# Kernel optimization log

Hardware: AMD Instinct MI355X
Metric: run time of the kernel (lower is better)

## Reference

```python
import jax, jax.numpy as jnp
import numpy as np

N_HEADS = 16
WINDOW = 4
THETA = 10000.0


def _freqs_1d(dim, L, theta=THETA):
    f = 1.0 / theta ** (np.arange(0, dim, 2, dtype=np.float32) / dim)  # [dim/2]
    ang = np.arange(L, dtype=np.float32)[:, None] * f[None, :]         # [L, dim/2]
    return jnp.asarray(np.cos(ang)), jnp.asarray(np.sin(ang))


def _freqs_2d(dim, H, W, theta=THETA):
    f = 1.0 / theta ** (np.arange(0, dim, 2, dtype=np.float32) / dim)  # [dim/2]
    fh = np.arange(H, dtype=np.float32)[:, None] * f[0::2][None, :]    # [H, dim/4]
    fw = np.arange(W, dtype=np.float32)[:, None] * f[1::2][None, :]    # [W, dim/4]
    ang = np.concatenate([
        np.broadcast_to(fh[:, None, :], (H, W, fh.shape[1])),
        np.broadcast_to(fw[None, :, :], (H, W, fw.shape[1])),
    ], axis=-1)                                                        # [H, W, dim/2]
    return jnp.asarray(np.cos(ang)), jnp.asarray(np.sin(ang))


def _rope(x, cos, sin):
    # x: [..., N, D]; cos/sin broadcastable to x's leading dims with trailing D/2
    sh = x.shape
    xr = x.reshape(sh[:-1] + (sh[-1] // 2, 2))
    re, im = xr[..., 0], xr[..., 1]
    o_re = re * cos - im * sin
    o_im = re * sin + im * cos
    return jnp.stack([o_re, o_im], axis=-1).reshape(sh)


def setup_inputs() -> dict:
    key = jax.random.key(0)
    ks = jax.random.split(key, 5)
    B, T, H, W, E = 2, 8, 16, 16, 512
    S = 2 * T * H * W
    std = 0.02
    return {
        "hidden_states": jax.random.normal(ks[0], (B, S, E), jnp.float32),
        "in_proj_weight": jax.random.normal(ks[1], (3 * E, E), jnp.float32) * std,
        "in_proj_bias": jnp.zeros((3 * E,), jnp.float32),
        "out_proj_weight": jax.random.normal(ks[2], (E, E), jnp.float32) * std,
        "out_proj_bias": jnp.zeros((E,), jnp.float32),
        "temporal_embed": jax.random.normal(ks[3], (WINDOW, E), jnp.float32) * std,
        "T": T, "H": H, "W": W,
    }


def reference(hidden_states, in_proj_weight, in_proj_bias, out_proj_weight,
              out_proj_bias, temporal_embed, T, H, W):
    B, S, E = hidden_states.shape
    n, d = N_HEADS, E // N_HEADS
    HW = H * W
    THW = T * HW
    L2 = 2 * HW  # tokens per frame fed to attention

    # first (outer) in-projection
    qkv = hidden_states @ in_proj_weight.T + in_proj_bias  # [B,S,3E]
    q, k, v = jnp.split(qkv, 3, axis=-1)
    q = q.reshape(B, S, n, d)
    k = k.reshape(B, S, n, d)

    # 1D RoPE on first T*H*W tokens (per-frame length H*W)
    cos1, sin1 = _freqs_1d(d, HW)
    c1, s1 = cos1[:, None, :], sin1[:, None, :]  # [HW,1,d/2]
    q1 = _rope(q[:, :THW].reshape(B * T, HW, n, d), c1, s1)
    k1 = _rope(k[:, :THW].reshape(B * T, HW, n, d), c1, s1)

    # 2D RoPE on last T*H*W tokens
    cos2, sin2 = _freqs_2d(d, H, W)
    c2, s2 = cos2[:, :, None, :], sin2[:, :, None, :]  # [H,W,1,d/2]
    q2 = _rope(q[:, THW:].reshape(B * T, H, W, n, d), c2, s2).reshape(B * T, HW, n, d)
    k2 = _rope(k[:, THW:].reshape(B * T, H, W, n, d), c2, s2).reshape(B * T, HW, n, d)

    q_mha = jnp.concatenate([q1, q2], axis=1).reshape(B * T, L2, E)
    k_comb = jnp.concatenate([k1, k2], axis=1).reshape(B, T, L2, E)
    v_comb = v.reshape(B, T, L2, E)

    # sliding window over frames (left-pad with zeros)
    k_pad = jnp.pad(k_comb, ((0, 0), (WINDOW - 1, 0), (0, 0), (0, 0)))
    v_pad = jnp.pad(v_comb, ((0, 0), (WINDOW - 1, 0), (0, 0), (0, 0)))
    k_win = jnp.stack([k_pad[:, i:i + T] for i in range(WINDOW)], axis=2)
    v_win = jnp.stack([v_pad[:, i:i + T] for i in range(WINDOW)], axis=2)
    k_win = k_win + temporal_embed[None, None, :, None, :]
    k_mha = k_win.reshape(B * T, WINDOW * L2, E)
    v_mha = v_win.reshape(B * T, WINDOW * L2, E)

    # inner nn.MultiheadAttention: projects q/k/v AGAIN with in_proj chunks
    Wq, Wk, Wv = jnp.split(in_proj_weight, 3, axis=0)
    bq, bk, bv = jnp.split(in_proj_bias, 3, axis=0)
    qh = (q_mha @ Wq.T + bq).reshape(B * T, L2, n, d)
    kh = (k_mha @ Wk.T + bk).reshape(B * T, WINDOW * L2, n, d)
    vh = (v_mha @ Wv.T + bv).reshape(B * T, WINDOW * L2, n, d)

    scale = 1.0 / jnp.sqrt(jnp.asarray(d, jnp.float32))
    scores = jnp.einsum('bqnd,bknd->bnqk', qh, kh) * scale
    attn = jax.nn.softmax(scores, axis=-1)
    o = jnp.einsum('bnqk,bknd->bqnd', attn, vh).reshape(B * T, L2, E)
    out = o @ out_proj_weight.T + out_proj_bias
    return out.reshape(B, S, E)
```

## Files before the change

### kernel.cpp

```cpp
#include <hip/hip_runtime.h>


#define LOG2T_OVER_16 0.83048202372184059f
#define SCL 0.25505837391169026f

typedef unsigned short u16;
typedef unsigned int u32;
typedef __attribute__((ext_vector_type(2))) unsigned int u32x2;
typedef __attribute__((ext_vector_type(4))) float f32x4;
typedef __attribute__((ext_vector_type(8))) short s16x8;

__device__ __forceinline__ u16 bf16b(float x) {
  u32 u = __float_as_uint(x);
  u32 r = u + 0x7FFFu + ((u >> 16) & 1u);
  return (u16)(r >> 16);
}
__device__ __forceinline__ float bf2f(u16 s) {
  return __uint_as_float(((u32)s) << 16);
}

__device__ __forceinline__ void gld_lds16(const u16* g, u16* l) {
  __builtin_amdgcn_global_load_lds(
      (const __attribute__((address_space(1))) unsigned int*)g,
      (__attribute__((address_space(3))) unsigned int*)l, 16, 0, 0);
}

__global__ __launch_bounds__(256) void cast_bf16(
    const float* __restrict__ src, u16* __restrict__ dst, int n8) {
  int i = blockIdx.x * 256 + threadIdx.x;
  if (i >= n8) return;
  float4 a = ((const float4*)src)[i * 2], b = ((const float4*)src)[i * 2 + 1];
  s16x8 w;
  w[0] = (short)bf16b(a.x); w[1] = (short)bf16b(a.y);
  w[2] = (short)bf16b(a.z); w[3] = (short)bf16b(a.w);
  w[4] = (short)bf16b(b.x); w[5] = (short)bf16b(b.y);
  w[6] = (short)bf16b(b.z); w[7] = (short)bf16b(b.w);
  ((s16x8*)dst)[i] = w;
}

template<int OUTF32>
__device__ __forceinline__ void gemm_core(
    const u16* __restrict__ A, const u16* __restrict__ Bw,
    const float* __restrict__ bias, void* __restrict__ Cp,
    int N, int K, float scale, u16* As, u16* Bs) {
  const int tid = threadIdx.x;
  const int row0 = blockIdx.y * 128;
  const int col0 = blockIdx.x * 128;
  const int lane = tid & 63, wid = tid >> 6;
  const int col = lane & 15, g = lane >> 4;
  const int wm = wid >> 1, wn = wid & 1;

  const int s0 = tid, s1 = 256 + tid;
  const int r0 = s0 >> 2, kp0 = (s0 & 3) * 8;
  const int r1 = s1 >> 2, kp1 = (s1 & 3) * 8;

  f32x4 acc[4][4] = {};

  auto stage = [&](int buf, int k0) {
    u16* ab = As + buf * 4096;
    u16* bb = Bs + buf * 4096;
    gld_lds16(A + (size_t)(row0 + r0) * K + k0 + kp0, ab + s0 * 8);
    gld_lds16(A + (size_t)(row0 + r1) * K + k0 + kp1, ab + s1 * 8);
    gld_lds16(Bw + (size_t)(col0 + r0) * K + k0 + kp0, bb + s0 * 8);
    gld_lds16(Bw + (size_t)(col0 + r1) * K + k0 + kp1, bb + s1 * 8);
  };

  stage(0, 0);
  asm volatile("s_waitcnt vmcnt(0)" ::: "memory");
  __syncthreads();

  const int NT = K / 32;
  int cur = 0;
  for (int t = 0; t < NT; ++t) {
    if (t + 1 < NT) stage(cur ^ 1, (t + 1) * 32);
    const u16* ab = As + cur * 4096;
    const u16* bb = Bs + cur * 4096;
    s16x8 a[4], b[4];
    #pragma unroll
    for (int i = 0; i < 4; ++i)
      a[i] = *(const s16x8*)(ab + (wm * 64 + i * 16 + col) * 32 + g * 8);
    #pragma unroll
    for (int i = 0; i < 4; ++i)
      b[i] = *(const s16x8*)(bb + (wn * 64 + i * 16 + col) * 32 + g * 8);
    #pragma unroll
    for (int mi = 0; mi < 4; ++mi)
      #pragma unroll
      for (int ni = 0; ni < 4; ++ni)
        acc[mi][ni] = __builtin_amdgcn_mfma_f32_16x16x32_bf16(a[mi], b[ni], acc[mi][ni], 0, 0, 0);
    asm volatile("s_waitcnt vmcnt(0)" ::: "memory");
    __syncthreads();
    cur ^= 1;
  }

  const int crow = row0 + wm * 64, ccol = col0 + wn * 64;
  #pragma unroll
  for (int mi = 0; mi < 4; ++mi) {
    #pragma unroll
    for (int ni = 0; ni < 4; ++ni) {
      const int cc = ccol + ni * 16 + col;
      const float bb_ = bias ? bias[cc] : 0.0f;
      #pragma unroll
      for (int r = 0; r < 4; ++r) {
        const int rr = crow + mi * 16 + g * 4 + r;
        float v = (acc[mi][ni][r] + bb_) * scale;
        if (OUTF32) ((float*)Cp)[(size_t)rr * N + cc] = v;
        else        ((u16*)Cp)[(size_t)rr * N + cc] = bf16b(v);
      }
    }
  }
}

__global__ __launch_bounds__(256) void gemm_bf16(
    const u16* __restrict__ A, const u16* __restrict__ Bw,
    const float* __restrict__ bias, u16* __restrict__ C, int N, int K, float scale) {
  __shared__ u16 As[2 * 4096];
  __shared__ u16 Bs[2 * 4096];
  gemm_core<0>(A, Bw, bias, C, N, K, scale, As, Bs);
}

__global__ __launch_bounds__(256) void gemm_f32out(
    const u16* __restrict__ A, const u16* __restrict__ Bw,
    const float* __restrict__ bias, float* __restrict__ C, int N, int K, float scale) {
  __shared__ u16 As[2 * 4096];
  __shared__ u16 Bs[2 * 4096];
  gemm_core<1>(A, Bw, bias, C, N, K, scale, As, Bs);
}

__global__ __launch_bounds__(256) void gemm2_batched(
    const u16* __restrict__ Ab, const u16* __restrict__ Wb,
    const float* __restrict__ b_in, u16* __restrict__ Cb) {
  __shared__ u16 As[2 * 4096];
  __shared__ u16 Bs[2 * 4096];
  const int z = blockIdx.z;
  const u16* A  = Ab + (size_t)z * 4194304;
  const u16* Bw = Wb + (size_t)z * 262144;
  u16* C = Cb + (size_t)z * 4194304;
  const float* bias = (z == 0) ? b_in : (z == 2 ? b_in + 1024 : nullptr);
  const float scale = (z == 0) ? SCL : 1.0f;
  gemm_core<0>(A, Bw, bias, C, 512, 512, scale, As, Bs);
}

__global__ __launch_bounds__(256) void rope_relayout_bf(
    const u16* __restrict__ qkv, u16* __restrict__ qm,
    u16* __restrict__ kc, u16* __restrict__ vc) {
  const int R = blockIdx.x * 2 + (threadIdx.x >> 7);
  const int t2 = threadIdx.x & 127;
  const int j = R & 511, bt = R >> 9;
  const int b = bt >> 3, tt = bt & 7;
  const int head = t2 >> 3, u0 = (t2 & 7) * 2;
  const int e0 = head * 32 + u0 * 2;

  float ang0, ang1; int tok;
  if (j < 256) {
    ang0 = (float)j * exp2f(-(float)u0 * LOG2T_OVER_16);
    ang1 = (float)j * exp2f(-(float)(u0 + 1) * LOG2T_OVER_16);
    tok = b * 4096 + tt * 256 + j;
  } else {
    const int jj = j - 256, hh = jj >> 4, ww = jj & 15;
    ang0 = (u0 < 8) ? (float)hh * exp2f(-(float)(2 * u0) * LOG2T_OVER_16)
                    : (float)ww * exp2f(-(float)(2 * (u0 - 8) + 1) * LOG2T_OVER_16);
    const int u1 = u0 + 1;
    ang1 = (u1 < 8) ? (float)hh * exp2f(-(float)(2 * u1) * LOG2T_OVER_16)
                    : (float)ww * exp2f(-(float)(2 * (u1 - 8) + 1) * LOG2T_OVER_16);
    tok = b * 4096 + 2048 + tt * 256 + jj;
  }
  float s0, c0, s1, c1;
  sincosf(ang0, &s0, &c0);
  sincosf(ang1, &s1, &c1);

  const size_t base = (size_t)tok * 1536 + e0;
  const size_t orow = (size_t)R * 512 + e0;

  auto rot = [&](u32x2 in) -> u32x2 {
    float r0 = bf2f((u16)(in[0] & 0xffff)), i0 = bf2f((u16)(in[0] >> 16));
    float r1 = bf2f((u16)(in[1] & 0xffff)), i1 = bf2f((u16)(in[1] >> 16));
    u32x2 o;
    o[0] = (u32)bf16b(r0 * c0 - i0 * s0) | ((u32)bf16b(r0 * s0 + i0 * c0) << 16);
    o[1] = (u32)bf16b(r1 * c1 - i1 * s1) | ((u32)bf16b(r1 * s1 + i1 * c1) << 16);
    return o;
  };
  *(u32x2*)(qm + orow) = rot(*(const u32x2*)(qkv + base));
  *(u32x2*)(kc + orow) = rot(*(const u32x2*)(qkv + base + 512));
  const int vtok = b * 4096 + tt * 512 + j;
  *(u32x2*)(vc + orow) = *(const u32x2*)(qkv + (size_t)vtok * 1536 + 1024 + e0);
}

__global__ __launch_bounds__(256) void tep_kernel(
    const float* __restrict__ te, const float* __restrict__ Wk,
    const float* __restrict__ bk, float* __restrict__ tep) {
  const int idx = blockIdx.x * 256 + threadIdx.x;
  const int i = idx >> 9, c = idx & 511;
  float s = bk[c];
  const float* terow = te + i * 512;
  const float* wrow = Wk + (size_t)c * 512;
  #pragma unroll 8
  for (int e = 0; e < 512; ++e) s = fmaf(terow[e], wrow[e], s);
  tep[idx] = s;
}

__global__ __launch_bounds__(256) void transpose_v_bf16(
    const u16* __restrict__ vc2, u16* __restrict__ vt) {
  const int f = blockIdx.x, h = blockIdx.y;
  __shared__ float tile[64][35];
  const int tid = threadIdx.x;
  for (int k0 = 0; k0 < 512; k0 += 64) {
    __syncthreads();
    {
      const int key = tid >> 2, d0 = (tid & 3) * 8;
      s16x8 v = *(const s16x8*)(vc2 + (size_t)(f * 512 + k0 + key) * 512 + h * 32 + d0);
      #pragma unroll
      for (int q = 0; q < 8; ++q) tile[key][d0 + q] = bf2f((u16)v[q]);
    }
    __syncthreads();
    {
      const int d = tid >> 3, j0 = (tid & 7) * 8;
      s16x8 w;
      #pragma unroll
      for (int q = 0; q < 8; ++q) w[q] = (short)bf16b(tile[j0 + q][d]);
      *(s16x8*)(vt + (size_t)((f * 16 + h) * 32 + d) * 512 + k0 + j0) = w;
    }
  }
}

__global__ __launch_bounds__(64, 2) void attn_mfma(
    const u16* __restrict__ qh, const u16* __restrict__ kbf,
    const float* __restrict__ tep, const u16* __restrict__ vt,
    const float* __restrict__ bv, u16* __restrict__ obf) {
  const int bt = blockIdx.x, h = blockIdx.y, zc = blockIdx.z;
  const int b = bt >> 3, t = bt & 7;
  const int lane = threadIdx.x;
  const int col = lane & 15, g = lane >> 4;

  __shared__ __align__(128) u16 plds[4096];
  const u32 plds_base = (u32)(uintptr_t)&plds[0] + (u32)lane * 8u;

  const int phys_e = (col & 4) ? 4 + (col >> 3) : (col >> 3);
  const int wbase = phys_e * 64 + (col & 3) * 16 + g * 4;

  const int qrow0 = bt * 512 + zc * 64;
  s16x8 qa[4];
  #pragma unroll
  for (int m = 0; m < 4; ++m)
    qa[m] = *(const s16x8*)(qh + (size_t)(qrow0 + m * 16 + col) * 512 + h * 32 + g * 8);

  f32x4 acc[4][2] = {};
  f32x4 lsum[4] = {};
  const f32x4 zero4 = {0.f, 0.f, 0.f, 0.f};

  for (int i = 0; i < 4; ++i) {
    const int fs = t + i - 3;
    const float* tprow = tep + i * 512 + h * 32;
    float t8[8];
    #pragma unroll
    for (int j = 0; j < 8; ++j) t8[j] = tprow[g * 8 + j];

    s16x8 kpad, vpad[2];
    if (fs < 0) {
      #pragma unroll
      for (int j = 0; j < 8; ++j) kpad[j] = (short)bf16b(t8[j]);
      #pragma unroll
      for (int n = 0; n < 2; ++n) {
        u16 vb = bf16b(bv[h * 32 + n * 16 + col]);
        #pragma unroll
        for (int j = 0; j < 8; ++j) vpad[n][j] = (short)vb;
      }
    }
    const int fsc = (fs < 0) ? 0 : fs;
    const size_t krow0 = (size_t)((b * 8 + fsc) * 512);
    const size_t vrow0 = (size_t)(((b * 8 + fsc) * 16 + h) * 32);

    for (int it = 0; it < 8; ++it) {
      const int kk0 = it * 64;
      f32x4 S[4][4];
      #pragma unroll
      for (int n = 0; n < 4; ++n) {
        s16x8 kb;
        if (fs >= 0) {
          s16x8 kv = *(const s16x8*)(kbf + (krow0 + kk0 + n * 16 + col) * 512 + h * 32 + g * 8);
          #pragma unroll
          for (int j = 0; j < 8; ++j)
            kb[j] = (short)bf16b(bf2f((u16)kv[j]) + t8[j]);
        } else {
          kb = kpad;
        }
        #pragma unroll
        for (int m = 0; m < 4; ++m)
          S[m][n] = __builtin_amdgcn_mfma_f32_16x16x32_bf16(qa[m], kb, zero4, 0, 0, 0);
      }
      #pragma unroll
      for (int m = 0; m < 4; ++m) {
        #pragma unroll
        for (int n = 0; n < 4; ++n) {
          f32x4 p;
          #pragma unroll
          for (int r = 0; r < 4; ++r) p[r] = __builtin_amdgcn_exp2f(S[m][n][r]);
          lsum[m] += p;
          u32 w0 = (u32)bf16b(p[0]) | ((u32)bf16b(p[1]) << 16);
          u32 w1 = (u32)bf16b(p[2]) | ((u32)bf16b(p[3]) << 16);
          const int E = m * 1024 + (n >> 1) * 512 + (n & 1) * 128 + wbase;
          *(uint2*)&plds[E] = make_uint2(w0, w1);
        }
      }
      s16x8 vfr[2][2];
      #pragma unroll
      for (int ks = 0; ks < 2; ++ks)
        #pragma unroll
        for (int n = 0; n < 2; ++n) {
          if (fs >= 0)
            vfr[ks][n] = *(const s16x8*)(vt + (vrow0 + n * 16 + col) * 512 + kk0 + ks * 32 + g * 8);
          else
            vfr[ks][n] = vpad[n];
        }
      asm volatile("s_waitcnt lgkmcnt(0)" ::: "memory");
      union AF { u32x2 h2[2]; s16x8 v; };
      AF pa[4][2];
      #pragma unroll
      for (int m = 0; m < 4; ++m)
        #pragma unroll
        for (int ks = 0; ks < 2; ++ks) {
          u32 a0 = plds_base + (u32)((m * 1024 + ks * 512) * 2);
          asm volatile("ds_read_b64_tr_b16 %0, %1" : "=v"(pa[m][ks].h2[0]) : "v"(a0));
          asm volatile("ds_read_b64_tr_b16 %0, %1 offset:512" : "=v"(pa[m][ks].h2[1]) : "v"(a0));
        }
      asm volatile("s_waitcnt lgkmcnt(0)" ::: "memory");
      __builtin_amdgcn_sched_barrier(0);
      #pragma unroll
      for (int m = 0; m < 4; ++m)
        #pragma unroll
        for (int ks = 0; ks < 2; ++ks)
          #pragma unroll
          for (int n = 0; n < 2; ++n)
            acc[m][n] = __builtin_amdgcn_mfma_f32_16x16x32_bf16(pa[m][ks].v, vfr[ks][n], acc[m][n], 0, 0, 0);
    }
  }

  #pragma unroll
  for (int m = 0; m < 4; ++m)
    #pragma unroll
    for (int r = 0; r < 4; ++r) {
      float s = lsum[m][r];
      s += __shfl_xor(s, 1);
      s += __shfl_xor(s, 2);
      s += __shfl_xor(s, 4);
      s += __shfl_xor(s, 8);
      lsum[m][r] = s;
    }

  #pragma unroll
  for (int m = 0; m < 4; ++m) {
    f32x4 inv;
    #pragma unroll
    for (int r = 0; r < 4; ++r) inv[r] = 1.0f / lsum[m][r];
    #pragma unroll
    for (int n = 0; n < 2; ++n)
      #pragma unroll
      for (int r = 0; r < 4; ++r)
        plds[(m * 16 + g * 4 + r) * 32 + n * 16 + col] = bf16b(acc[m][n][r] * inv[r]);
  }
  asm volatile("s_waitcnt lgkmcnt(0)" ::: "memory");
  #pragma unroll
  for (int i = 0; i < 8; ++i) {
    const int row = i * 8 + (lane >> 3);
    u32x2 w = *(u32x2*)&plds[row * 32 + (lane & 7) * 4];
    *(u32x2*)(obf + (size_t)(qrow0 + row) * 512 + h * 32 + (lane & 7) * 4) = w;
  }
}

extern "C" void kernel_launch(void* const* d_in, const int* in_sizes, int n_in,
                              void* d_out, int out_size, void* d_ws, size_t ws_size,
                              hipStream_t stream) {
  (void)in_sizes; (void)n_in; (void)out_size; (void)ws_size;
  const float* hs    = (const float*)d_in[0];
  const float* w_in  = (const float*)d_in[1];
  const float* b_in  = (const float*)d_in[2];
  const float* w_out = (const float*)d_in[3];
  const float* b_out = (const float*)d_in[4];
  const float* te    = (const float*)d_in[5];

  u16* w16 = (u16*)d_ws;
  u16* hs_bf   = w16;
  u16* win_bf  = w16 + 4194304;
  u16* wout_bf = w16 + 4980736;
  u16* qkv_bf  = w16 + 5242880;
  u16* qm_bf   = w16 + 17825792;
  u16* kc_bf   = w16 + 22020096;
  u16* vc_bf   = w16 + 26214400;
  float* tep   = (float*)(w16 + 30408704);
  u16* qh_bf   = w16 + 5242880;
  u16* kbf     = w16 + 9437184;
  u16* vc2_bf  = w16 + 13631488;
  u16* vt      = w16 + 17825792;
  u16* o_bf    = w16 + 22020096;

  cast_bf16<<<4194304 / 8 / 256, 256, 0, stream>>>(hs, hs_bf, 4194304 / 8);
  cast_bf16<<<786432 / 8 / 256, 256, 0, stream>>>(w_in, win_bf, 786432 / 8);
  cast_bf16<<<262144 / 8 / 256, 256, 0, stream>>>(w_out, wout_bf, 262144 / 8);

  gemm_bf16<<<dim3(12, 64), 256, 0, stream>>>(hs_bf, win_bf, b_in, qkv_bf, 1536, 512, 1.0f);

  rope_relayout_bf<<<4096, 256, 0, stream>>>(qkv_bf, qm_bf, kc_bf, vc_bf);

  tep_kernel<<<8, 256, 0, stream>>>(te, w_in + 512 * 512, b_in + 512, tep);

  gemm2_batched<<<dim3(4, 64, 3), 256, 0, stream>>>(qm_bf, win_bf, b_in, qh_bf);

  transpose_v_bf16<<<dim3(16, 16), 256, 0, stream>>>(vc2_bf, vt);

  attn_mfma<<<dim3(16, 16, 8), 64, 0, stream>>>(qh_bf, kbf, tep, vt, b_in + 1024, o_bf);

  gemm_f32out<<<dim3(4, 64), 256, 0, stream>>>(o_bf, wout_bf, b_out, (float*)d_out, 512, 512, 1.0f);
}
```

Before: 299.3 us.

## Split attention window frames across waves, shortcut padded frames, tabulate RoPE angles

```diff
diff --git a/kernel.cpp b/kernel.cpp
--- a/kernel.cpp
+++ b/kernel.cpp
@@ -18,6 +18,11 @@
 __device__ __forceinline__ float bf2f(u16 s) {
   return __uint_as_float(((u32)s) << 16);
 }
+__device__ __forceinline__ u32 cvtpk(float lo, float hi) {
+  u32 r;
+  asm("v_cvt_pk_bf16_f32 %0, %1, %2" : "=v"(r) : "v"(lo), "v"(hi));
+  return r;
+}
 
 __device__ __forceinline__ void gld_lds16(const u16* g, u16* l) {
   __builtin_amdgcn_global_load_lds(
@@ -30,12 +35,10 @@
   int i = blockIdx.x * 256 + threadIdx.x;
   if (i >= n8) return;
   float4 a = ((const float4*)src)[i * 2], b = ((const float4*)src)[i * 2 + 1];
-  s16x8 w;
-  w[0] = (short)bf16b(a.x); w[1] = (short)bf16b(a.y);
-  w[2] = (short)bf16b(a.z); w[3] = (short)bf16b(a.w);
-  w[4] = (short)bf16b(b.x); w[5] = (short)bf16b(b.y);
-  w[6] = (short)bf16b(b.z); w[7] = (short)bf16b(b.w);
-  ((s16x8*)dst)[i] = w;
+  union { u32 u[4]; s16x8 v; } w;
+  w.u[0] = cvtpk(a.x, a.y); w.u[1] = cvtpk(a.z, a.w);
+  w.u[2] = cvtpk(b.x, b.y); w.u[3] = cvtpk(b.z, b.w);
+  ((s16x8*)dst)[i] = w.v;
 }
 
 template<int OUTF32>
@@ -140,9 +143,25 @@
   gemm_core<0>(A, Bw, bias, C, 512, 512, scale, As, Bs);
 }
 
+__global__ __launch_bounds__(256) void ang_table_kernel(float2* __restrict__ tab) {
+  const int idx = blockIdx.x * 256 + threadIdx.x;
+  const int j = idx >> 4, u = idx & 15;
+  float ang;
+  if (j < 256) {
+    ang = (float)j * exp2f(-(float)u * LOG2T_OVER_16);
+  } else {
+    const int jj = j - 256, hh = jj >> 4, ww = jj & 15;
+    ang = (u < 8) ? (float)hh * exp2f(-(float)(2 * u) * LOG2T_OVER_16)
+                  : (float)ww * exp2f(-(float)(2 * (u - 8) + 1) * LOG2T_OVER_16);
+  }
+  float s, c;
+  sincosf(ang, &s, &c);
+  tab[idx] = make_float2(c, s);
+}
+
 __global__ __launch_bounds__(256) void rope_relayout_bf(
-    const u16* __restrict__ qkv, u16* __restrict__ qm,
-    u16* __restrict__ kc, u16* __restrict__ vc) {
+    const u16* __restrict__ qkv, const float2* __restrict__ tab,
+    u16* __restrict__ qm, u16* __restrict__ kc, u16* __restrict__ vc) {
   const int R = blockIdx.x * 2 + (threadIdx.x >> 7);
   const int t2 = threadIdx.x & 127;
   const int j = R & 511, bt = R >> 9;
@@ -150,23 +169,10 @@
   const int head = t2 >> 3, u0 = (t2 & 7) * 2;
   const int e0 = head * 32 + u0 * 2;
 
-  float ang0, ang1; int tok;
-  if (j < 256) {
-    ang0 = (float)j * exp2f(-(float)u0 * LOG2T_OVER_16);
-    ang1 = (float)j * exp2f(-(float)(u0 + 1) * LOG2T_OVER_16);
-    tok = b * 4096 + tt * 256 + j;
-  } else {
-    const int jj = j - 256, hh = jj >> 4, ww = jj & 15;
-    ang0 = (u0 < 8) ? (float)hh * exp2f(-(float)(2 * u0) * LOG2T_OVER_16)
-                    : (float)ww * exp2f(-(float)(2 * (u0 - 8) + 1) * LOG2T_OVER_16);
-    const int u1 = u0 + 1;
-    ang1 = (u1 < 8) ? (float)hh * exp2f(-(float)(2 * u1) * LOG2T_OVER_16)
-                    : (float)ww * exp2f(-(float)(2 * (u1 - 8) + 1) * LOG2T_OVER_16);
-    tok = b * 4096 + 2048 + tt * 256 + jj;
-  }
-  float s0, c0, s1, c1;
-  sincosf(ang0, &s0, &c0);
-  sincosf(ang1, &s1, &c1);
+  const int tok = (j < 256) ? (b * 4096 + tt * 256 + j)
+                            : (b * 4096 + 2048 + tt * 256 + (j - 256));
+  float4 cs = *(const float4*)&tab[j * 16 + u0];
+  const float c0 = cs.x, s0 = cs.y, c1 = cs.z, s1 = cs.w;
 
   const size_t base = (size_t)tok * 1536 + e0;
   const size_t orow = (size_t)R * 512 + e0;
@@ -175,8 +181,8 @@
     float r0 = bf2f((u16)(in[0] & 0xffff)), i0 = bf2f((u16)(in[0] >> 16));
     float r1 = bf2f((u16)(in[1] & 0xffff)), i1 = bf2f((u16)(in[1] >> 16));
     u32x2 o;
-    o[0] = (u32)bf16b(r0 * c0 - i0 * s0) | ((u32)bf16b(r0 * s0 + i0 * c0) << 16);
-    o[1] = (u32)bf16b(r1 * c1 - i1 * s1) | ((u32)bf16b(r1 * s1 + i1 * c1) << 16);
+    o[0] = cvtpk(r0 * c0 - i0 * s0, r0 * s0 + i0 * c0);
+    o[1] = cvtpk(r1 * c1 - i1 * s1, r1 * s1 + i1 * c1);
     return o;
   };
   *(u32x2*)(qm + orow) = rot(*(const u32x2*)(qkv + base));
@@ -214,25 +220,29 @@
     __syncthreads();
     {
       const int d = tid >> 3, j0 = (tid & 7) * 8;
-      s16x8 w;
-      #pragma unroll
-      for (int q = 0; q < 8; ++q) w[q] = (short)bf16b(tile[j0 + q][d]);
-      *(s16x8*)(vt + (size_t)((f * 16 + h) * 32 + d) * 512 + k0 + j0) = w;
-    }
-  }
-}
-
-__global__ __launch_bounds__(64, 2) void attn_mfma(
+      union { u32 u[4]; s16x8 v; } w;
+      #pragma unroll
+      for (int q = 0; q < 4; ++q)
+        w.u[q] = cvtpk(tile[j0 + 2 * q][d], tile[j0 + 2 * q + 1][d]);
+      *(s16x8*)(vt + (size_t)((f * 16 + h) * 32 + d) * 512 + k0 + j0) = w.v;
+    }
+  }
+}
+
+__global__ __launch_bounds__(256) void attn_mfma(
     const u16* __restrict__ qh, const u16* __restrict__ kbf,
     const float* __restrict__ tep, const u16* __restrict__ vt,
     const float* __restrict__ bv, u16* __restrict__ obf) {
   const int bt = blockIdx.x, h = blockIdx.y, zc = blockIdx.z;
   const int b = bt >> 3, t = bt & 7;
-  const int lane = threadIdx.x;
+  const int tid = threadIdx.x;
+  const int lane = tid & 63, w = tid >> 6;
   const int col = lane & 15, g = lane >> 4;
 
-  __shared__ __align__(128) u16 plds[4096];
-  const u32 plds_base = (u32)(uintptr_t)&plds[0] + (u32)lane * 8u;
+  __shared__ __align__(128) u16 plds[4][4096];
+  u16* pl = plds[w];
+  const u32 pl_base = (u32)(uintptr_t)pl + (u32)lane * 8u;
+  float* cf = (float*)&plds[0][0];
 
   const int phys_e = (col & 4) ? 4 + (col >> 3) : (col >> 3);
   const int wbase = phys_e * 64 + (col & 3) * 16 + g * 4;
@@ -247,45 +257,52 @@
   f32x4 lsum[4] = {};
   const f32x4 zero4 = {0.f, 0.f, 0.f, 0.f};
 
-  for (int i = 0; i < 4; ++i) {
-    const int fs = t + i - 3;
-    const float* tprow = tep + i * 512 + h * 32;
-    float t8[8];
-    #pragma unroll
-    for (int j = 0; j < 8; ++j) t8[j] = tprow[g * 8 + j];
-
-    s16x8 kpad, vpad[2];
-    if (fs < 0) {
-      #pragma unroll
-      for (int j = 0; j < 8; ++j) kpad[j] = (short)bf16b(t8[j]);
-      #pragma unroll
-      for (int n = 0; n < 2; ++n) {
-        u16 vb = bf16b(bv[h * 32 + n * 16 + col]);
-        #pragma unroll
-        for (int j = 0; j < 8; ++j) vpad[n][j] = (short)vb;
+  const int fs = t + w - 3;
+  const float* tprow = tep + w * 512 + h * 32;
+  float t8[8];
+  #pragma unroll
+  for (int j = 0; j < 8; ++j) t8[j] = tprow[g * 8 + j];
+
+  if (fs < 0) {
+    float* pf = (float*)pl;
+    #pragma unroll
+    for (int m = 0; m < 4; ++m) {
+      float part = 0.f;
+      #pragma unroll
+      for (int j = 0; j < 8; ++j) part = fmaf(bf2f((u16)qa[m][j]), t8[j], part);
+      part += __shfl_xor(part, 16);
+      part += __shfl_xor(part, 32);
+      float e = __builtin_amdgcn_exp2f(part) * 512.0f;
+      if (lane < 16) pf[m * 16 + col] = e;
+    }
+    asm volatile("s_waitcnt lgkmcnt(0)" ::: "memory");
+    const float bv0 = bv[h * 32 + col], bv1 = bv[h * 32 + 16 + col];
+    #pragma unroll
+    for (int m = 0; m < 4; ++m)
+      #pragma unroll
+      for (int r = 0; r < 4; ++r) {
+        float e = pf[m * 16 + g * 4 + r];
+        lsum[m][r] += (col == 0) ? e : 0.f;
+        acc[m][0][r] += e * bv0;
+        acc[m][1][r] += e * bv1;
       }
-    }
-    const int fsc = (fs < 0) ? 0 : fs;
-    const size_t krow0 = (size_t)((b * 8 + fsc) * 512);
-    const size_t vrow0 = (size_t)(((b * 8 + fsc) * 16 + h) * 32);
-
+  } else {
+    const size_t krow0 = (size_t)((b * 8 + fs) * 512);
+    const size_t vrow0 = (size_t)(((b * 8 + fs) * 16 + h) * 32);
     for (int it = 0; it < 8; ++it) {
       const int kk0 = it * 64;
       f32x4 S[4][4];
       #pragma unroll
       for (int n = 0; n < 4; ++n) {
-        s16x8 kb;
-        if (fs >= 0) {
-          s16x8 kv = *(const s16x8*)(kbf + (krow0 + kk0 + n * 16 + col) * 512 + h * 32 + g * 8);
-          #pragma unroll
-          for (int j = 0; j < 8; ++j)
-            kb[j] = (short)bf16b(bf2f((u16)kv[j]) + t8[j]);
-        } else {
-          kb = kpad;
-        }
+        s16x8 kv = *(const s16x8*)(kbf + (krow0 + kk0 + n * 16 + col) * 512 + h * 32 + g * 8);
+        union { u32 u[4]; s16x8 v; } kb;
+        #pragma unroll
+        for (int p = 0; p < 4; ++p)
+          kb.u[p] = cvtpk(bf2f((u16)kv[2 * p]) + t8[2 * p],
+                          bf2f((u16)kv[2 * p + 1]) + t8[2 * p + 1]);
         #pragma unroll
         for (int m = 0; m < 4; ++m)
-          S[m][n] = __builtin_amdgcn_mfma_f32_16x16x32_bf16(qa[m], kb, zero4, 0, 0, 0);
+          S[m][n] = __builtin_amdgcn_mfma_f32_16x16x32_bf16(qa[m], kb.v, zero4, 0, 0, 0);
       }
       #pragma unroll
       for (int m = 0; m < 4; ++m) {
@@ -295,22 +312,16 @@
           #pragma unroll
           for (int r = 0; r < 4; ++r) p[r] = __builtin_amdgcn_exp2f(S[m][n][r]);
           lsum[m] += p;
-          u32 w0 = (u32)bf16b(p[0]) | ((u32)bf16b(p[1]) << 16);
-          u32 w1 = (u32)bf16b(p[2]) | ((u32)bf16b(p[3]) << 16);
           const int E = m * 1024 + (n >> 1) * 512 + (n & 1) * 128 + wbase;
-          *(uint2*)&plds[E] = make_uint2(w0, w1);
+          *(uint2*)&pl[E] = make_uint2(cvtpk(p[0], p[1]), cvtpk(p[2], p[3]));
         }
       }
       s16x8 vfr[2][2];
       #pragma unroll
       for (int ks = 0; ks < 2; ++ks)
         #pragma unroll
-        for (int n = 0; n < 2; ++n) {
-          if (fs >= 0)
-            vfr[ks][n] = *(const s16x8*)(vt + (vrow0 + n * 16 + col) * 512 + kk0 + ks * 32 + g * 8);
-          else
-            vfr[ks][n] = vpad[n];
-        }
+        for (int n = 0; n < 2; ++n)
+          vfr[ks][n] = *(const s16x8*)(vt + (vrow0 + n * 16 + col) * 512 + kk0 + ks * 32 + g * 8);
       asm volatile("s_waitcnt lgkmcnt(0)" ::: "memory");
       union AF { u32x2 h2[2]; s16x8 v; };
       AF pa[4][2];
@@ -318,7 +329,7 @@
       for (int m = 0; m < 4; ++m)
         #pragma unroll
         for (int ks = 0; ks < 2; ++ks) {
-          u32 a0 = plds_base + (u32)((m * 1024 + ks * 512) * 2);
+          u32 a0 = pl_base + (u32)((m * 1024 + ks * 512) * 2);
           asm volatile("ds_read_b64_tr_b16 %0, %1" : "=v"(pa[m][ks].h2[0]) : "v"(a0));
           asm volatile("ds_read_b64_tr_b16 %0, %1 offset:512" : "=v"(pa[m][ks].h2[1]) : "v"(a0));
         }
@@ -346,23 +357,51 @@
       lsum[m][r] = s;
     }
 
-  #pragma unroll
-  for (int m = 0; m < 4; ++m) {
-    f32x4 inv;
-    #pragma unroll
-    for (int r = 0; r < 4; ++r) inv[r] = 1.0f / lsum[m][r];
-    #pragma unroll
-    for (int n = 0; n < 2; ++n)
-      #pragma unroll
-      for (int r = 0; r < 4; ++r)
-        plds[(m * 16 + g * 4 + r) * 32 + n * 16 + col] = bf16b(acc[m][n][r] * inv[r]);
-  }
-  asm volatile("s_waitcnt lgkmcnt(0)" ::: "memory");
-  #pragma unroll
-  for (int i = 0; i < 8; ++i) {
-    const int row = i * 8 + (lane >> 3);
-    u32x2 w = *(u32x2*)&plds[row * 32 + (lane & 7) * 4];
-    *(u32x2*)(obf + (size_t)(qrow0 + row) * 512 + h * 32 + (lane & 7) * 4) = w;
+  __syncthreads();
+  if (w > 0) {
+    float* dst = cf + (size_t)(w - 1) * 2048 + lane * 32;
+    #pragma unroll
+    for (int m = 0; m < 4; ++m) {
+      *(f32x4*)(dst + m * 8) = acc[m][0];
+      *(f32x4*)(dst + m * 8 + 4) = acc[m][1];
+    }
+    if (col == 0) {
+      float* d2 = cf + 6144 + (w - 1) * 64 + g * 16;
+      #pragma unroll
+      for (int m = 0; m < 4; ++m) *(f32x4*)(d2 + m * 4) = lsum[m];
+    }
+  }
+  __syncthreads();
+  if (w == 0) {
+    #pragma unroll
+    for (int w2 = 0; w2 < 3; ++w2) {
+      const float* src = cf + (size_t)w2 * 2048 + lane * 32;
+      const float* s2 = cf + 6144 + w2 * 64 + g * 16;
+      #pragma unroll
+      for (int m = 0; m < 4; ++m) {
+        acc[m][0] += *(const f32x4*)(src + m * 8);
+        acc[m][1] += *(const f32x4*)(src + m * 8 + 4);
+        lsum[m] += *(const f32x4*)(s2 + m * 4);
+      }
+    }
+    #pragma unroll
+    for (int m = 0; m < 4; ++m) {
+      f32x4 inv;
+      #pragma unroll
+      for (int r = 0; r < 4; ++r) inv[r] = 1.0f / lsum[m][r];
+      #pragma unroll
+      for (int n = 0; n < 2; ++n)
+        #pragma unroll
+        for (int r = 0; r < 4; ++r)
+          pl[(m * 16 + g * 4 + r) * 32 + n * 16 + col] = bf16b(acc[m][n][r] * inv[r]);
+    }
+    asm volatile("s_waitcnt lgkmcnt(0)" ::: "memory");
+    #pragma unroll
+    for (int i = 0; i < 8; ++i) {
+      const int row = i * 8 + (lane >> 3);
+      u32x2 wv = *(u32x2*)&pl[row * 32 + (lane & 7) * 4];
+      *(u32x2*)(obf + (size_t)(qrow0 + row) * 512 + h * 32 + (lane & 7) * 4) = wv;
+    }
   }
 }
 
@@ -386,6 +425,7 @@
   u16* kc_bf   = w16 + 22020096;
   u16* vc_bf   = w16 + 26214400;
   float* tep   = (float*)(w16 + 30408704);
+  float2* tab  = (float2*)(w16 + 30412800);
   u16* qh_bf   = w16 + 5242880;
   u16* kbf     = w16 + 9437184;
   u16* vc2_bf  = w16 + 13631488;
@@ -395,10 +435,11 @@
   cast_bf16<<<4194304 / 8 / 256, 256, 0, stream>>>(hs, hs_bf, 4194304 / 8);
   cast_bf16<<<786432 / 8 / 256, 256, 0, stream>>>(w_in, win_bf, 786432 / 8);
   cast_bf16<<<262144 / 8 / 256, 256, 0, stream>>>(w_out, wout_bf, 262144 / 8);
+  ang_table_kernel<<<32, 256, 0, stream>>>(tab);
 
   gemm_bf16<<<dim3(12, 64), 256, 0, stream>>>(hs_bf, win_bf, b_in, qkv_bf, 1536, 512, 1.0f);
 
-  rope_relayout_bf<<<4096, 256, 0, stream>>>(qkv_bf, qm_bf, kc_bf, vc_bf);
+  rope_relayout_bf<<<4096, 256, 0, stream>>>(qkv_bf, tab, qm_bf, kc_bf, vc_bf);
 
   tep_kernel<<<8, 256, 0, stream>>>(te, w_in + 512 * 512, b_in + 512, tep);
 
@@ -406,7 +447,7 @@
 
   transpose_v_bf16<<<dim3(16, 16), 256, 0, stream>>>(vc2_bf, vt);
 
-  attn_mfma<<<dim3(16, 16, 8), 64, 0, stream>>>(qh_bf, kbf, tep, vt, b_in + 1024, o_bf);
+  attn_mfma<<<dim3(16, 16, 8), 256, 0, stream>>>(qh_bf, kbf, tep, vt, b_in + 1024, o_bf);
 
   gemm_f32out<<<dim3(4, 64), 256, 0, stream>>>(o_bf, wout_bf, b_out, (float*)d_out, 512, 512, 1.0f);
 }
```

Measured after the change: 281.3 us. 1.06x faster.
